# Kernel tuning notes

Measured on AMD Instinct MI355X. Metric: run time of the kernel, lower is better.

Reference implementation:

```python
import jax, jax.numpy as jnp
import numpy as np

N_NODES = 100_000
N_EDGES = 3_200_000
VOCAB = 50_000
D = 256
L_GNN = 4
L_LIN = 2
OUT = 10          # label_size=10 -> output_size=10
N_TGT = 8192
EPS = 1e-5


def layer_norm(x, g, b):
    mu = jnp.mean(x, axis=-1, keepdims=True)
    var = jnp.mean((x - mu) ** 2, axis=-1, keepdims=True)
    return (x - mu) * jax.lax.rsqrt(var + EPS) * g + b


def gcn_conv(x, src, dst, W, b, n):
    # PyG GCNConv defaults: add self loops, symmetric D^-1/2 (A+I) D^-1/2 norm
    h = x @ W                                   # [n, D]
    loops = jnp.arange(n, dtype=src.dtype)
    src2 = jnp.concatenate([src, loops])        # [E+n]
    dst2 = jnp.concatenate([dst, loops])
    deg = jax.ops.segment_sum(jnp.ones(src2.shape[0], dtype=h.dtype), dst2, n)
    dinv = jnp.where(deg > 0, jax.lax.rsqrt(deg), 0.0)
    norm = dinv[src2] * dinv[dst2]              # [E+n]
    out = jax.ops.segment_sum(h[src2] * norm[:, None], dst2, n)  # [n, D]
    return out + b


def setup_inputs() -> dict:
    key = jax.random.key(0)
    ks = jax.random.split(key, 16)
    tokens = jax.random.randint(ks[0], (N_NODES,), 0, VOCAB, dtype=jnp.int32)
    edges = jax.random.randint(ks[1], (2, N_EDGES), 0, N_NODES, dtype=jnp.int32)
    target_indices = jax.random.randint(ks[2], (N_TGT,), 0, N_NODES, dtype=jnp.int32)
    s = 0.05
    emb_table = jax.random.normal(ks[3], (VOCAB, D), jnp.float32)
    gnn_W = jax.random.normal(ks[4], (L_GNN, D, D), jnp.float32) * s
    gnn_b = jnp.zeros((L_GNN, D), jnp.float32)
    gnn_gamma = jnp.ones((L_GNN, D), jnp.float32)
    gnn_beta = jnp.zeros((L_GNN, D), jnp.float32)
    lin_W = jax.random.normal(ks[5], (L_LIN, D, D), jnp.float32) * s
    lin_b = jnp.zeros((L_LIN, D), jnp.float32)
    lin_gamma = jnp.ones((L_LIN, D), jnp.float32)
    lin_beta = jnp.zeros((L_LIN, D), jnp.float32)
    out_W = jax.random.normal(ks[6], (D, OUT), jnp.float32) * s
    out_b = jnp.zeros((OUT,), jnp.float32)
    return {"tokens": tokens, "edges": edges, "target_indices": target_indices,
            "emb_table": emb_table, "gnn_W": gnn_W, "gnn_b": gnn_b,
            "gnn_gamma": gnn_gamma, "gnn_beta": gnn_beta,
            "lin_W": lin_W, "lin_b": lin_b, "lin_gamma": lin_gamma,
            "lin_beta": lin_beta, "out_W": out_W, "out_b": out_b}


def reference(tokens, edges, target_indices, emb_table, gnn_W, gnn_b,
              gnn_gamma, gnn_beta, lin_W, lin_b, lin_gamma, lin_beta,
              out_W, out_b):
    x = emb_table[tokens]                       # [N, D] embedding lookup
    src, dst = edges[0], edges[1]
    for i in range(L_GNN):
        x = gcn_conv(x, src, dst, gnn_W[i], gnn_b[i], N_NODES)
        x = layer_norm(x, gnn_gamma[i], gnn_beta[i])
        x = jax.nn.relu(x)
    x = x[target_indices]                       # [N_TGT, D]
    for i in range(L_LIN):
        x = x @ lin_W[i] + lin_b[i]
        x = layer_norm(x, lin_gamma[i], lin_beta[i])
        x = jax.nn.relu(x)
    return x @ out_W + out_b                    # [N_TGT, OUT]
```

## Files before the change

kernel.cpp:

```cpp
#include <hip/hip_runtime.h>
#include <hip/hip_fp16.h>

#define NN 100000
#define NE 3200000
#define DD 256
#define NT 8192
#define NOUT 10
#define NBUCK 196
#define CSRP_CAP (NE + NBUCK * 4112 + 64)

typedef unsigned short u16;
typedef unsigned int u32;
typedef unsigned char u8;
typedef __attribute__((ext_vector_type(8))) short bf16x8;
typedef __attribute__((ext_vector_type(4))) float f32x4;
typedef __attribute__((ext_vector_type(4))) unsigned int uint4v;

__device__ __forceinline__ float bf2f(u16 u) {
    union { unsigned int i; float f; } v; v.i = ((unsigned int)u) << 16; return v.f;
}
__device__ __forceinline__ u16 f2bf(float f) {
    union { float f; unsigned int i; } v; v.f = f;
    unsigned int x = v.i;
    return (u16)((x + 0x7fffu + ((x >> 16) & 1u)) >> 16);
}
__device__ __forceinline__ unsigned int pack2(float a, float b) {
    return (unsigned int)f2bf(a) | ((unsigned int)f2bf(b) << 16);
}

__device__ __forceinline__ void gl2lds16(const void* g, void* l) {
    __builtin_amdgcn_global_load_lds(
        (const __attribute__((address_space(1))) unsigned int*)g,
        (__attribute__((address_space(3))) unsigned int*)l, 16, 0, 0);
}

__global__ __launch_bounds__(256) void k_wt(const float* __restrict__ gW,
                                            const float* __restrict__ lW,
                                            u16* __restrict__ Wt,
                                            int* __restrict__ bucketCnt,
                                            float* __restrict__ tq) {
    if (blockIdx.x == 0 && threadIdx.x < NBUCK) bucketCnt[threadIdx.x] = 0;
    if (blockIdx.x == 0 && threadIdx.x < 4) tq[NN * 4 + threadIdx.x] = 0.0f;
    int idx = blockIdx.x * 256 + threadIdx.x;
    int l = idx >> 16;
    int nk = idx & 65535;
    int n = nk >> 8, k = nk & 255;
    float v = (l < 4) ? gW[l * 65536 + k * 256 + n]
                      : lW[(l - 4) * 65536 + k * 256 + n];
    Wt[idx] = f2bf(v);
}

__global__ __launch_bounds__(256) void k_binA(const int* __restrict__ dst,
                                              int* __restrict__ bucketCnt) {
    __shared__ int hist[NBUCK];
    int t = threadIdx.x;
    if (t < NBUCK) hist[t] = 0;
    __syncthreads();
    int base = blockIdx.x * 4096;
#pragma unroll
    for (int i = 0; i < 16; i++) {
        int e = base + i * 256 + t;
        if (e < NE) atomicAdd(&hist[dst[e] >> 9], 1);
    }
    __syncthreads();
    if (t < NBUCK && hist[t] > 0) atomicAdd(&bucketCnt[t], hist[t]);
}

__global__ __launch_bounds__(256) void k_bscan(const int* __restrict__ bucketCnt,
                                               int* __restrict__ bucketOff,
                                               int* __restrict__ bucketCur) {
    __shared__ int s[256];
    int t = threadIdx.x;
    int v = (t < NBUCK) ? bucketCnt[t] : 0;
    s[t] = v;
    __syncthreads();
    for (int o = 1; o < 256; o <<= 1) {
        int a = (t >= o) ? s[t - o] : 0;
        __syncthreads();
        s[t] += a;
        __syncthreads();
    }
    if (t < NBUCK) {
        int ex = s[t] - v;
        bucketOff[t] = ex;
        bucketCur[t] = ex;
    }
    if (t == 0) bucketOff[NBUCK] = NE;
}

__global__ __launch_bounds__(1024) void k_binB(const int* __restrict__ src,
                                               const int* __restrict__ dst,
                                               int* __restrict__ bucketCur,
                                               int* __restrict__ recs) {
    __shared__ int hist[NBUCK];
    __shared__ int gbase[NBUCK];
    int t = threadIdx.x;
    if (t < NBUCK) hist[t] = 0;
    __syncthreads();
    int base = blockIdx.x * 16384;
    int recv[16], bks[16], rnk[16];
#pragma unroll
    for (int i = 0; i < 16; i++) {
        int e = base + i * 1024 + t;
        int bk = -1, rec = 0;
        if (e < NE) {
            int s_ = src[e], d_ = dst[e];
            bk = d_ >> 9;
            rec = (s_ << 9) | (d_ & 511);
        }
        bks[i] = bk; recv[i] = rec;
    }
#pragma unroll
    for (int i = 0; i < 16; i++)
        rnk[i] = (bks[i] >= 0) ? atomicAdd(&hist[bks[i]], 1) : 0;
    __syncthreads();
    if (t < NBUCK) {
        int c = hist[t];
        gbase[t] = (c > 0) ? atomicAdd(&bucketCur[t], c) : 0;
    }
    __syncthreads();
#pragma unroll
    for (int i = 0; i < 16; i++)
        if (bks[i] >= 0) {
            int pos = gbase[bks[i]] + rnk[i];
            pos = min(max(pos, 0), NE - 1);
            recs[pos] = recv[i];
        }
}

__global__ __launch_bounds__(256) void k_csrA(const int* __restrict__ recs,
                                              const int* __restrict__ bucketOff,
                                              int2* __restrict__ nodeInfo,
                                              float* __restrict__ dinv,
                                              u32* __restrict__ csrp) {
    __shared__ int cnt[512], off[512];
    int b = blockIdx.x, t = threadIdx.x;
    int beg = min(max(bucketOff[b], 0), NE);
    int end = min(max(bucketOff[b + 1], beg), NE);
    int n = end - beg;
    cnt[t] = 0; cnt[t + 256] = 0;
    __syncthreads();
    for (int i = t; i < n; i += 256)
        atomicAdd(&cnt[recs[beg + i] & 511], 1);
    __syncthreads();
    off[t] = (cnt[t] + 8) & ~7;
    off[t + 256] = (cnt[t + 256] + 8) & ~7;
    __syncthreads();
    for (int o = 1; o < 512; o <<= 1) {
        int v0 = (t >= o) ? off[t - o] : 0;
        int v1 = (t + 256 >= o) ? off[t + 256 - o] : 0;
        __syncthreads();
        off[t] += v0; off[t + 256] += v1;
        __syncthreads();
    }
    int base = (beg + b * 4112 + 7) & ~7;
    for (int k = t; k < 512; k += 256) {
        int node = b * 512 + k;
        if (node >= NN) continue;
        int pd = (cnt[k] + 8) & ~7;
        int nbeg = base + off[k] - pd;
        int2 ni; ni.x = nbeg; ni.y = pd;
        nodeInfo[node] = ni;
        dinv[node] = rsqrtf((float)(cnt[k] + 1));
        csrp[nbeg] = (u32)node;
        for (int j = nbeg + 1 + cnt[k]; j < nbeg + pd; j++) csrp[j] = (u32)NN;
    }
}

__global__ __launch_bounds__(256) void k_csrB(const int* __restrict__ recs,
                                              const int* __restrict__ bucketOff,
                                              const int2* __restrict__ nodeInfo,
                                              u32* __restrict__ csrp) {
    __shared__ int cur[512];
    int b = blockIdx.x, t = threadIdx.x;
    cur[t] = 0; cur[t + 256] = 0;
    __syncthreads();
    int beg = min(max(bucketOff[b], 0), NE);
    int end = min(max(bucketOff[b + 1], beg), NE);
    int n = end - beg;
    for (int i = t; i < n; i += 256) {
        int r = recs[beg + i];
        int dlow = r & 511;
        int s = min(max(r >> 9, 0), NN - 1);
        int node = b * 512 + dlow;
        int rk = atomicAdd(&cur[dlow], 1);
        int2 ni = nodeInfo[node];
        int pos = ni.x + 1 + rk;
        pos = min(max(pos, 0), CSRP_CAP - 1);
        csrp[pos] = (u32)s;
    }
}

#define GEMM_EPILOGUE                                                         \
    for (int i = 0; i < 4; i++)                                               \
        for (int j = 0; j < 4; j++) {                                         \
            int col = colBase + wn * 64 + j * 16 + l16;                       \
            for (int r = 0; r < 4; r++) {                                     \
                int row = rowBase + wm * 64 + i * 16 + quad * 4 + r;          \
                if (row < M) C[row * 256 + col] = f2bf(acc[i][j][r]);         \
            }                                                                 \
        }

#define GEMM_COMPUTE(ASRC, BSRC)                                              \
    for (int ks = 0; ks < 2; ks++) {                                          \
        bf16x8 a_frag[4], b_frag[4];                                          \
        for (int i = 0; i < 4; i++) {                                         \
            int r = wm * 64 + i * 16 + l16;                                   \
            int ch = (ks * 4 + quad) ^ (r & 7);                               \
            a_frag[i] = *(const bf16x8*)(&ASRC[r * 64 + ch * 8]);             \
        }                                                                     \
        for (int j = 0; j < 4; j++) {                                         \
            int r = wn * 64 + j * 16 + l16;                                   \
            int ch = (ks * 4 + quad) ^ (r & 7);                               \
            b_frag[j] = *(const bf16x8*)(&BSRC[r * 64 + ch * 8]);             \
        }                                                                     \
        for (int i = 0; i < 4; i++)                                           \
            for (int j = 0; j < 4; j++)                                       \
                acc[i][j] = __builtin_amdgcn_mfma_f32_16x16x32_bf16(          \
                    a_frag[i], b_frag[j], acc[i][j], 0, 0, 0);                \
    }

#define QUANT_EPILOGUE(Q8, TQ)                                                \
    {                                                                         \
        u8* bb = (u8*)As;                          \
        const int gq = blockIdx.y * 2 + wn;                                   \
        for (int i = 0; i < 4; i++) {                                         \
            float m0 = 0.f, m1 = 0.f, m2 = 0.f, m3 = 0.f;                     \
            for (int j = 0; j < 4; j++) {                                     \
                m0 = fmaxf(m0, fabsf(acc[i][j][0]));                          \
                m1 = fmaxf(m1, fabsf(acc[i][j][1]));                          \
                m2 = fmaxf(m2, fabsf(acc[i][j][2]));                          \
                m3 = fmaxf(m3, fabsf(acc[i][j][3]));                          \
            }                                                                 \
            for (int o = 1; o < 16; o <<= 1) {                                \
                m0 = fmaxf(m0, __shfl_xor(m0, o, 64));                        \
                m1 = fmaxf(m1, __shfl_xor(m1, o, 64));                        \
                m2 = fmaxf(m2, __shfl_xor(m2, o, 64));                        \
                m3 = fmaxf(m3, __shfl_xor(m3, o, 64));                        \
            }                                                                 \
            float i0 = m0 > 0.f ? 126.f / m0 : 0.f;                           \
            float i1 = m1 > 0.f ? 126.f / m1 : 0.f;                           \
            float i2 = m2 > 0.f ? 126.f / m2 : 0.f;                           \
            float i3 = m3 > 0.f ? 126.f / m3 : 0.f;                           \
            int row0 = rowBase + wm * 64 + i * 16 + quad * 4;                 \
            if (l16 == 0) {                                                   \
                if (row0 + 0 < M)                                             \
                    TQ[(row0+0)*4+gq] = m0 * (1.f/126.f) * dinv[row0+0];      \
                if (row0 + 1 < M)                                             \
                    TQ[(row0+1)*4+gq] = m1 * (1.f/126.f) * dinv[row0+1];      \
                if (row0 + 2 < M)                                             \
                    TQ[(row0+2)*4+gq] = m2 * (1.f/126.f) * dinv[row0+2];      \
                if (row0 + 3 < M)                                             \
                    TQ[(row0+3)*4+gq] = m3 * (1.f/126.f) * dinv[row0+3];      \
            }                                                                 \
            int rb = (wm * 64 + i * 16 + quad * 4) * 128;                     \
            for (int j = 0; j < 4; j++) {                                     \
                int cb = wn * 64 + j * 16 + l16;                              \
                bb[rb + cb]       = (u8)((int)rintf(acc[i][j][0]*i0) + 128);  \
                bb[rb + 128 + cb] = (u8)((int)rintf(acc[i][j][1]*i1) + 128);  \
                bb[rb + 256 + cb] = (u8)((int)rintf(acc[i][j][2]*i2) + 128);  \
                bb[rb + 384 + cb] = (u8)((int)rintf(acc[i][j][3]*i3) + 128);  \
            }                                                                 \
        }                                                                     \
        __syncthreads();                                                      \
        for (int u = tid; u < 1024; u += 256) {                               \
            int r = u >> 3, c16 = (u & 7) * 16;                               \
            int row = rowBase + r;                                            \
            if (row < M)                                                      \
                *(uint4*)(Q8 + (size_t)row * 256 + colBase + c16) =           \
                    *(const uint4*)(bb + r * 128 + c16);                      \
        }                                                                     \
    }

__global__ __launch_bounds__(256) void k_gemm(const u16* __restrict__ A,
                                              const u16* __restrict__ Bt,
                                              u16* __restrict__ C, int M) {
    __shared__ __align__(16) u16 As[128 * 64];
    __shared__ __align__(16) u16 Bs[128 * 64];
    const int tid = threadIdx.x;
    const int wave = tid >> 6, lane = tid & 63;
    const int wm = wave >> 1, wn = wave & 1;
    const int rowBase = blockIdx.x * 128;
    const int colBase = blockIdx.y * 128;
    const int quad = lane >> 4, l16 = lane & 15;

    f32x4 acc[4][4] = {};

    for (int kk = 0; kk < 4; kk++) {
        int k0 = kk * 64;
#pragma unroll
        for (int i = 0; i < 4; i++) {
            int j = (i * 4 + wave) * 64 + lane;
            int r = j >> 3, c = j & 7;
            int cg = c ^ (r & 7);
            int ga = rowBase + r; if (ga >= M) ga = M - 1;
            gl2lds16(A + (size_t)ga * 256 + k0 + cg * 8,
                     &As[(i * 4 + wave) * 512]);
            gl2lds16(Bt + (size_t)(colBase + r) * 256 + k0 + cg * 8,
                     &Bs[(i * 4 + wave) * 512]);
        }
        __syncthreads();
        GEMM_COMPUTE(As, Bs)
        __syncthreads();
    }
    GEMM_EPILOGUE
}

__global__ __launch_bounds__(256) void k_gemmq(const u16* __restrict__ A,
                                               const u16* __restrict__ Bt,
                                               const float* __restrict__ dinv,
                                               u8* __restrict__ q8,
                                               float* __restrict__ tq, int M) {
    __shared__ __align__(16) u16 As[128 * 64];
    __shared__ __align__(16) u16 Bs[128 * 64];
    const int tid = threadIdx.x;
    const int wave = tid >> 6, lane = tid & 63;
    const int wm = wave >> 1, wn = wave & 1;
    const int rowBase = blockIdx.x * 128;
    const int colBase = blockIdx.y * 128;
    const int quad = lane >> 4, l16 = lane & 15;

    f32x4 acc[4][4] = {};

    for (int kk = 0; kk < 4; kk++) {
        int k0 = kk * 64;
#pragma unroll
        for (int i = 0; i < 4; i++) {
            int j = (i * 4 + wave) * 64 + lane;
            int r = j >> 3, c = j & 7;
            int cg = c ^ (r & 7);
            int ga = rowBase + r; if (ga >= M) ga = M - 1;
            gl2lds16(A + (size_t)ga * 256 + k0 + cg * 8,
                     &As[(i * 4 + wave) * 512]);
            gl2lds16(Bt + (size_t)(colBase + r) * 256 + k0 + cg * 8,
                     &Bs[(i * 4 + wave) * 512]);
        }
        __syncthreads();
        GEMM_COMPUTE(As, Bs)
        __syncthreads();
    }
    QUANT_EPILOGUE(q8, tq)
}

__global__ __launch_bounds__(256) void k_gemm_embq(const int* __restrict__ tokens,
                                                   const float* __restrict__ emb,
                                                   const u16* __restrict__ Bt,
                                                   const float* __restrict__ dinv,
                                                   u8* __restrict__ q8,
                                                   float* __restrict__ tq, int M) {
    __shared__ __align__(16) u16 As[128 * 64];
    __shared__ __align__(16) u16 Bs[128 * 64];
    __shared__ int tokLDS[128];
    const int tid = threadIdx.x;
    const int wave = tid >> 6, lane = tid & 63;
    const int wm = wave >> 1, wn = wave & 1;
    const int rowBase = blockIdx.x * 128;
    const int colBase = blockIdx.y * 128;
    const int quad = lane >> 4, l16 = lane & 15;

    if (tid < 128) {
        int ga = rowBase + tid; if (ga >= M) ga = M - 1;
        tokLDS[tid] = tokens[ga];
    }
    f32x4 acc[4][4] = {};
    __syncthreads();

    for (int kk = 0; kk < 4; kk++) {
        int k0 = kk * 64;
#pragma unroll
        for (int i = 0; i < 4; i++) {
            int j = (i * 4 + wave) * 64 + lane;
            int r = j >> 3, c = j & 7;
            int cg = c ^ (r & 7);
            const float* srcp = emb + (size_t)tokLDS[r] * 256 + k0 + cg * 8;
            float4 f0 = *(const float4*)srcp;
            float4 f1 = *(const float4*)(srcp + 4);
            uint4 pk;
            pk.x = pack2(f0.x, f0.y); pk.y = pack2(f0.z, f0.w);
            pk.z = pack2(f1.x, f1.y); pk.w = pack2(f1.z, f1.w);
            *(uint4*)(&As[j * 8]) = pk;
            gl2lds16(Bt + (size_t)(colBase + r) * 256 + k0 + cg * 8,
                     &Bs[(i * 4 + wave) * 512]);
        }
        __syncthreads();
        GEMM_COMPUTE(As, Bs)
        __syncthreads();
    }
    QUANT_EPILOGUE(q8, tq)
}

__global__ __launch_bounds__(256) void k_gemm_gather(const u16* __restrict__ X,
                                                     const int* __restrict__ tgt,
                                                     const u16* __restrict__ Bt,
                                                     u16* __restrict__ C, int M) {
    __shared__ __align__(16) u16 As[128 * 64];
    __shared__ __align__(16) u16 Bs[128 * 64];
    __shared__ int rowLDS[128];
    const int tid = threadIdx.x;
    const int wave = tid >> 6, lane = tid & 63;
    const int wm = wave >> 1, wn = wave & 1;
    const int rowBase = blockIdx.x * 128;
    const int colBase = blockIdx.y * 128;
    const int quad = lane >> 4, l16 = lane & 15;

    if (tid < 128) {
        int ga = rowBase + tid; if (ga >= M) ga = M - 1;
        rowLDS[tid] = tgt[ga];
    }
    f32x4 acc[4][4] = {};
    __syncthreads();

    for (int kk = 0; kk < 4; kk++) {
        int k0 = kk * 64;
#pragma unroll
        for (int i = 0; i < 4; i++) {
            int j = (i * 4 + wave) * 64 + lane;
            int r = j >> 3, c = j & 7;
            int cg = c ^ (r & 7);
            uint4 v = *(const uint4*)(X + (size_t)rowLDS[r] * 256 + k0 + cg * 8);
            *(uint4*)(&As[j * 8]) = v;
            gl2lds16(Bt + (size_t)(colBase + r) * 256 + k0 + cg * 8,
                     &Bs[(i * 4 + wave) * 512]);
        }
        __syncthreads();
        GEMM_COMPUTE(As, Bs)
        __syncthreads();
    }
    GEMM_EPILOGUE
}

#define GF8(RR, Q0, Q1, Q2, Q3, W0, W1, W2, W3)                               \
    {                                                                         \
        int s0 = (int)RR.x, s1 = (int)RR.y, s2 = (int)RR.z, s3 = (int)RR.w;   \
        Q0 = *(const uint2*)(qb + (size_t)s0 * 256);                          \
        Q1 = *(const uint2*)(qb + (size_t)s1 * 256);                          \
        Q2 = *(const uint2*)(qb + (size_t)s2 * 256);                          \
        Q3 = *(const uint2*)(qb + (size_t)s3 * 256);                          \
        W0 = tq[s0 * 4 + sg4]; W1 = tq[s1 * 4 + sg4];                         \
        W2 = tq[s2 * 4 + sg4]; W3 = tq[s3 * 4 + sg4];                         \
    }

#define GC8_ONE(Q, W)                                                         \
    {                                                                         \
        Ks += W;                                                              \
        a0 = fmaf(W, (float)(Q.x & 255u), a0);                                \
        a1 = fmaf(W, (float)((Q.x >> 8) & 255u), a1);                         \
        a2 = fmaf(W, (float)((Q.x >> 16) & 255u), a2);                        \
        a3 = fmaf(W, (float)(Q.x >> 24), a3);                                 \
        a4 = fmaf(W, (float)(Q.y & 255u), a4);                                \
        a5 = fmaf(W, (float)((Q.y >> 8) & 255u), a5);                         \
        a6 = fmaf(W, (float)((Q.y >> 16) & 255u), a6);                        \
        a7 = fmaf(W, (float)(Q.y >> 24), a7);                                 \
    }

__global__ __launch_bounds__(256) void k_aggr(const u8* __restrict__ q8,
                                              const float* __restrict__ tq,
                                              const float* __restrict__ dinv,
                                              const int2* __restrict__ nodeInfo,
                                              const u32* __restrict__ csrp,
                                              const float* __restrict__ bias,
                                              const float* __restrict__ gamma,
                                              const float* __restrict__ beta,
                                              u16* __restrict__ xo) {
    const int wave = threadIdx.x >> 6, lane = threadIdx.x & 63;
    const int half = lane >> 5, l32 = lane & 31;
    const int node = blockIdx.x * 4 + wave;
    const int d8 = l32 * 8;
    const int sg4 = l32 >> 3;
    int2 ni = nodeInfo[node];
    float a0=0,a1=0,a2=0,a3=0,a4=0,a5=0,a6=0,a7=0;
    float Ks = 0.0f;
    const u8* qb = q8 + d8;
    const u32* cp = csrp + ni.x + half * 4;
    const int nrec = ni.y;
    int j = 0;
    for (; j + 16 <= nrec; j += 16, cp += 16) {
        uint4v ra = __builtin_nontemporal_load((const uint4v*)cp);
        uint4v rb = __builtin_nontemporal_load((const uint4v*)(cp + 8));
        uint2 qa0, qa1, qa2, qa3, qb0, qb1, qb2, qb3;
        float wa0, wa1, wa2, wa3, wb0, wb1, wb2, wb3;
        GF8(ra, qa0, qa1, qa2, qa3, wa0, wa1, wa2, wa3);
        GF8(rb, qb0, qb1, qb2, qb3, wb0, wb1, wb2, wb3);
        GC8_ONE(qa0, wa0); GC8_ONE(qa1, wa1);
        GC8_ONE(qa2, wa2); GC8_ONE(qa3, wa3);
        GC8_ONE(qb0, wb0); GC8_ONE(qb1, wb1);
        GC8_ONE(qb2, wb2); GC8_ONE(qb3, wb3);
    }
    if (j < nrec) {
        uint4v ra = __builtin_nontemporal_load((const uint4v*)cp);
        uint2 qa0, qa1, qa2, qa3;
        float wa0, wa1, wa2, wa3;
        GF8(ra, qa0, qa1, qa2, qa3, wa0, wa1, wa2, wa3);
        GC8_ONE(qa0, wa0); GC8_ONE(qa1, wa1);
        GC8_ONE(qa2, wa2); GC8_ONE(qa3, wa3);
    }
    a0 += __shfl_xor(a0, 32, 64); a1 += __shfl_xor(a1, 32, 64);
    a2 += __shfl_xor(a2, 32, 64); a3 += __shfl_xor(a3, 32, 64);
    a4 += __shfl_xor(a4, 32, 64); a5 += __shfl_xor(a5, 32, 64);
    a6 += __shfl_xor(a6, 32, 64); a7 += __shfl_xor(a7, 32, 64);
    Ks += __shfl_xor(Ks, 32, 64);

    float dv = dinv[node];
    float c128 = 128.0f * Ks;
    float4 b0 = *(const float4*)(bias + d8);
    float4 b1 = *(const float4*)(bias + d8 + 4);
    a0 = (a0 - c128) * dv + b0.x; a1 = (a1 - c128) * dv + b0.y;
    a2 = (a2 - c128) * dv + b0.z; a3 = (a3 - c128) * dv + b0.w;
    a4 = (a4 - c128) * dv + b1.x; a5 = (a5 - c128) * dv + b1.y;
    a6 = (a6 - c128) * dv + b1.z; a7 = (a7 - c128) * dv + b1.w;
    float s1 = a0+a1+a2+a3+a4+a5+a6+a7;
    float s2 = a0*a0+a1*a1+a2*a2+a3*a3+a4*a4+a5*a5+a6*a6+a7*a7;
    for (int o = 16; o >= 1; o >>= 1) {
        s1 += __shfl_xor(s1, o, 64);
        s2 += __shfl_xor(s2, o, 64);
    }
    float mean = s1 * (1.0f / 256.0f);
    float var = s2 * (1.0f / 256.0f) - mean * mean;
    float rstd = rsqrtf(var + 1e-5f);
    if (half == 0) {
        float4 g0 = *(const float4*)(gamma + d8);
        float4 g1 = *(const float4*)(gamma + d8 + 4);
        float4 e0 = *(const float4*)(beta + d8);
        float4 e1 = *(const float4*)(beta + d8 + 4);
        float y0 = fmaxf((a0 - mean) * rstd * g0.x + e0.x, 0.0f);
        float y1 = fmaxf((a1 - mean) * rstd * g0.y + e0.y, 0.0f);
        float y2 = fmaxf((a2 - mean) * rstd * g0.z + e0.z, 0.0f);
        float y3 = fmaxf((a3 - mean) * rstd * g0.w + e0.w, 0.0f);
        float y4 = fmaxf((a4 - mean) * rstd * g1.x + e1.x, 0.0f);
        float y5 = fmaxf((a5 - mean) * rstd * g1.y + e1.y, 0.0f);
        float y6 = fmaxf((a6 - mean) * rstd * g1.z + e1.z, 0.0f);
        float y7 = fmaxf((a7 - mean) * rstd * g1.w + e1.w, 0.0f);
        uint4v o;
        o.x = pack2(y0, y1);
        o.y = pack2(y2, y3);
        o.z = pack2(y4, y5);
        o.w = pack2(y6, y7);
        __builtin_nontemporal_store(o, (uint4v*)(xo + node * 256 + d8));
    }
}

__global__ __launch_bounds__(256) void k_lnrelu(const u16* __restrict__ h,
                                                const float* __restrict__ bias,
                                                const float* __restrict__ gamma,
                                                const float* __restrict__ beta,
                                                u16* __restrict__ xo) {
    int wave = threadIdx.x >> 6, lane = threadIdx.x & 63;
    int row = blockIdx.x * 4 + wave;
    int base = row * 256 + lane * 4;
    ushort4 hv = *(const ushort4*)(h + base);
    float4 bv = *(const float4*)(bias + lane * 4);
    float a0 = bf2f(hv.x) + bv.x, a1 = bf2f(hv.y) + bv.y;
    float a2 = bf2f(hv.z) + bv.z, a3 = bf2f(hv.w) + bv.w;
    float s1 = a0 + a1 + a2 + a3;
    float s2 = a0 * a0 + a1 * a1 + a2 * a2 + a3 * a3;
    for (int o = 32; o >= 1; o >>= 1) {
        s1 += __shfl_xor(s1, o, 64);
        s2 += __shfl_xor(s2, o, 64);
    }
    float mean = s1 * (1.0f / 256.0f);
    float var = s2 * (1.0f / 256.0f) - mean * mean;
    float rstd = rsqrtf(var + 1e-5f);
    float4 gv = *(const float4*)(gamma + lane * 4);
    float4 be = *(const float4*)(beta + lane * 4);
    float y0 = fmaxf((a0 - mean) * rstd * gv.x + be.x, 0.0f);
    float y1 = fmaxf((a1 - mean) * rstd * gv.y + be.y, 0.0f);
    float y2 = fmaxf((a2 - mean) * rstd * gv.z + be.z, 0.0f);
    float y3 = fmaxf((a3 - mean) * rstd * gv.w + be.w, 0.0f);
    ushort4 o4;
    o4.x = f2bf(y0); o4.y = f2bf(y1); o4.z = f2bf(y2); o4.w = f2bf(y3);
    *(ushort4*)(xo + base) = o4;
}

__global__ __launch_bounds__(256) void k_lnout(const u16* __restrict__ h,
                                               const float* __restrict__ bias,
                                               const float* __restrict__ gamma,
                                               const float* __restrict__ beta,
                                               const float* __restrict__ W,
                                               const float* __restrict__ ob,
                                               float* __restrict__ out) {
    __shared__ float Ws[DD * NOUT];
    int tid = threadIdx.x;
    for (int i = tid; i < DD * NOUT; i += 256) Ws[i] = W[i];
    __syncthreads();
    int wave = tid >> 6, lane = tid & 63;
    int row = blockIdx.x * 4 + wave;
    int base = row * 256 + lane * 4;
    ushort4 hv = *(const ushort4*)(h + base);
    float4 bv = *(const float4*)(bias + lane * 4);
    float a0 = bf2f(hv.x) + bv.x, a1 = bf2f(hv.y) + bv.y;
    float a2 = bf2f(hv.z) + bv.z, a3 = bf2f(hv.w) + bv.w;
    float s1 = a0 + a1 + a2 + a3;
    float s2 = a0 * a0 + a1 * a1 + a2 * a2 + a3 * a3;
    for (int o = 32; o >= 1; o >>= 1) {
        s1 += __shfl_xor(s1, o, 64);
        s2 += __shfl_xor(s2, o, 64);
    }
    float mean = s1 * (1.0f / 256.0f);
    float var = s2 * (1.0f / 256.0f) - mean * mean;
    float rstd = rsqrtf(var + 1e-5f);
    float4 gv = *(const float4*)(gamma + lane * 4);
    float4 be = *(const float4*)(beta + lane * 4);
    float y0 = bf2f(f2bf(fmaxf((a0 - mean) * rstd * gv.x + be.x, 0.0f)));
    float y1 = bf2f(f2bf(fmaxf((a1 - mean) * rstd * gv.y + be.y, 0.0f)));
    float y2 = bf2f(f2bf(fmaxf((a2 - mean) * rstd * gv.z + be.z, 0.0f)));
    float y3 = bf2f(f2bf(fmaxf((a3 - mean) * rstd * gv.w + be.w, 0.0f)));
    int d = lane * 4;
    for (int o = 0; o < NOUT; o++) {
        float p = y0 * Ws[(d + 0) * NOUT + o] + y1 * Ws[(d + 1) * NOUT + o] +
                  y2 * Ws[(d + 2) * NOUT + o] + y3 * Ws[(d + 3) * NOUT + o];
        for (int off = 32; off >= 1; off >>= 1) p += __shfl_xor(p, off, 64);
        if (lane == 0) out[row * NOUT + o] = p + ob[o];
    }
}

extern "C" void kernel_launch(void* const* d_in, const int* in_sizes, int n_in,
                              void* d_out, int out_size, void* d_ws, size_t ws_size,
                              hipStream_t stream) {
    (void)in_sizes; (void)n_in; (void)out_size; (void)ws_size;
    const int* tokens = (const int*)d_in[0];
    const int* edges = (const int*)d_in[1];
    const int* tgt = (const int*)d_in[2];
    const float* emb = (const float*)d_in[3];
    const float* gnn_W = (const float*)d_in[4];
    const float* gnn_b = (const float*)d_in[5];
    const float* gnn_g = (const float*)d_in[6];
    const float* gnn_be = (const float*)d_in[7];
    const float* lin_W = (const float*)d_in[8];
    const float* lin_b = (const float*)d_in[9];
    const float* lin_g = (const float*)d_in[10];
    const float* lin_be = (const float*)d_in[11];
    const float* out_W = (const float*)d_in[12];
    const float* out_b = (const float*)d_in[13];
    float* out = (float*)d_out;

    char* ws = (char*)d_ws;
    u16* x = (u16*)ws;           ws += (size_t)NN * 256 * 2;
    char* hreg = ws;             ws += (size_t)NN * 256 * 2;
    int* recs = (int*)hreg;
    u32* csrp = (u32*)ws;        ws += (size_t)CSRP_CAP * 4;
    int2* nodeInfo = (int2*)ws;  ws += (size_t)NN * 8;
    float* dinv = (float*)ws;    ws += (size_t)NN * 4;
    int* bucketCnt = (int*)ws;   ws += 256 * 4;
    int* bucketOff = (int*)ws;   ws += 256 * 4;
    int* bucketCur = (int*)ws;   ws += 256 * 4;
    u16* Wt = (u16*)ws;          ws += (size_t)6 * 65536 * 2;
    u16* xt = (u16*)ws;          ws += (size_t)NT * 256 * 2;
    u16* ht = (u16*)ws;          ws += (size_t)NT * 256 * 2;
    u8* q8 = (u8*)ws;            ws += (size_t)(NN + 8) * 256;
    float* tq = (float*)ws;      ws += (size_t)(NN + 1) * 16;

    const int* e_src = edges;
    const int* e_dst = edges + NE;

    k_wt<<<1536, 256, 0, stream>>>(gnn_W, lin_W, Wt, bucketCnt, tq);
    k_binA<<<782, 256, 0, stream>>>(e_dst, bucketCnt);
    k_bscan<<<1, 256, 0, stream>>>(bucketCnt, bucketOff, bucketCur);
    k_binB<<<196, 1024, 0, stream>>>(e_src, e_dst, bucketCur, recs);
    k_csrA<<<NBUCK, 256, 0, stream>>>(recs, bucketOff, nodeInfo, dinv, csrp);
    k_csrB<<<NBUCK, 256, 0, stream>>>(recs, bucketOff, nodeInfo, csrp);

    for (int l = 0; l < 4; l++) {
        if (l == 0)
            k_gemm_embq<<<dim3(782, 2), 256, 0, stream>>>(tokens, emb, Wt,
                                                          dinv, q8, tq, NN);
        else
            k_gemmq<<<dim3(782, 2), 256, 0, stream>>>(x, Wt + l * 65536,
                                                      dinv, q8, tq, NN);
        k_aggr<<<25000, 256, 0, stream>>>(q8, tq, dinv, nodeInfo, csrp,
                                          gnn_b + l * 256, gnn_g + l * 256,
                                          gnn_be + l * 256, x);
    }
    k_gemm_gather<<<dim3(64, 2), 256, 0, stream>>>(x, tgt, Wt + 4 * 65536,
                                                   ht, NT);
    k_lnrelu<<<2048, 256, 0, stream>>>(ht, lin_b, lin_g, lin_be, xt);
    k_gemm<<<dim3(64, 2), 256, 0, stream>>>(xt, Wt + 5 * 65536, ht, NT);
    k_lnout<<<2048, 256, 0, stream>>>(ht, lin_b + 256, lin_g + 256,
                                      lin_be + 256, out_W, out_b, out);
}
```

Measured before the change: 1.110 ms.

## Pack fp16 edge norm weights into CSR records and split quant scales per group

Each CSR record now holds the source index in the high 17 bits and a 15-bit fp16 symmetric-normalisation weight dinv[src]*dinv[dst] in the low bits. This removes the dinv multiply in the aggregation epilogue and the per-row dinv folding in the GEMM quant epilogue. Per-row quant scales move from an interleaved [N,4] layout to four planar [4,N] arrays, so each lane group reads its own plane. Padding records become zero-weight entries that point at node 0 instead of a dummy zero row. The trade is fp16 precision on edge weights, plus an extra random dinv[src] read during CSR build.

```diff
diff --git a/kernel.cpp b/kernel.cpp
--- a/kernel.cpp
+++ b/kernel.cpp
@@ -27,6 +27,13 @@
 __device__ __forceinline__ unsigned int pack2(float a, float b) {
     return (unsigned int)f2bf(a) | ((unsigned int)f2bf(b) << 16);
 }
+__device__ __forceinline__ u32 packrec(int src, float w) {
+    unsigned short h = __half_as_ushort(__float2half(w));
+    return ((u32)src << 15) | (u32)(h & 0x7fff);
+}
+__device__ __forceinline__ float recw(u32 r) {
+    return __half2float(__ushort_as_half((unsigned short)(r & 0x7fff)));
+}
 
 __device__ __forceinline__ void gl2lds16(const void* g, void* l) {
     __builtin_amdgcn_global_load_lds(
@@ -37,10 +44,8 @@
 __global__ __launch_bounds__(256) void k_wt(const float* __restrict__ gW,
                                             const float* __restrict__ lW,
                                             u16* __restrict__ Wt,
-                                            int* __restrict__ bucketCnt,
-                                            float* __restrict__ tq) {
+                                            int* __restrict__ bucketCnt) {
     if (blockIdx.x == 0 && threadIdx.x < NBUCK) bucketCnt[threadIdx.x] = 0;
-    if (blockIdx.x == 0 && threadIdx.x < 4) tq[NN * 4 + threadIdx.x] = 0.0f;
     int idx = blockIdx.x * 256 + threadIdx.x;
     int l = idx >> 16;
     int nk = idx & 65535;
@@ -161,15 +166,17 @@
         int nbeg = base + off[k] - pd;
         int2 ni; ni.x = nbeg; ni.y = pd;
         nodeInfo[node] = ni;
-        dinv[node] = rsqrtf((float)(cnt[k] + 1));
-        csrp[nbeg] = (u32)node;
-        for (int j = nbeg + 1 + cnt[k]; j < nbeg + pd; j++) csrp[j] = (u32)NN;
+        float di = rsqrtf((float)(cnt[k] + 1));
+        dinv[node] = di;
+        csrp[nbeg] = packrec(node, di * di);
+        for (int j = nbeg + 1 + cnt[k]; j < nbeg + pd; j++) csrp[j] = 0u;
     }
 }
 
 __global__ __launch_bounds__(256) void k_csrB(const int* __restrict__ recs,
                                               const int* __restrict__ bucketOff,
                                               const int2* __restrict__ nodeInfo,
+                                              const float* __restrict__ dinv,
                                               u32* __restrict__ csrp) {
     __shared__ int cur[512];
     int b = blockIdx.x, t = threadIdx.x;
@@ -185,9 +192,10 @@
         int node = b * 512 + dlow;
         int rk = atomicAdd(&cur[dlow], 1);
         int2 ni = nodeInfo[node];
+        float w = dinv[s] * dinv[node];
         int pos = ni.x + 1 + rk;
         pos = min(max(pos, 0), CSRP_CAP - 1);
-        csrp[pos] = (u32)s;
+        csrp[pos] = packrec(s, w);
     }
 }
 
@@ -220,10 +228,11 @@
                     a_frag[i], b_frag[j], acc[i][j], 0, 0, 0);                \
     }
 
-#define QUANT_EPILOGUE(Q8, TQ)                                                \
+#define QUANT_EPILOGUE(Q8, QS)                                                \
     {                                                                         \
         u8* bb = (u8*)As;                          \
         const int gq = blockIdx.y * 2 + wn;                                   \
+        float* qsp = QS + (size_t)gq * NN;                                    \
         for (int i = 0; i < 4; i++) {                                         \
             float m0 = 0.f, m1 = 0.f, m2 = 0.f, m3 = 0.f;                     \
             for (int j = 0; j < 4; j++) {                                     \
@@ -244,14 +253,10 @@
             float i3 = m3 > 0.f ? 126.f / m3 : 0.f;                           \
             int row0 = rowBase + wm * 64 + i * 16 + quad * 4;                 \
             if (l16 == 0) {                                                   \
-                if (row0 + 0 < M)                                             \
-                    TQ[(row0+0)*4+gq] = m0 * (1.f/126.f) * dinv[row0+0];      \
-                if (row0 + 1 < M)                                             \
-                    TQ[(row0+1)*4+gq] = m1 * (1.f/126.f) * dinv[row0+1];      \
-                if (row0 + 2 < M)                                             \
-                    TQ[(row0+2)*4+gq] = m2 * (1.f/126.f) * dinv[row0+2];      \
-                if (row0 + 3 < M)                                             \
-                    TQ[(row0+3)*4+gq] = m3 * (1.f/126.f) * dinv[row0+3];      \
+                if (row0 + 0 < M) qsp[row0 + 0] = m0 * (1.f / 126.f);         \
+                if (row0 + 1 < M) qsp[row0 + 1] = m1 * (1.f / 126.f);         \
+                if (row0 + 2 < M) qsp[row0 + 2] = m2 * (1.f / 126.f);         \
+                if (row0 + 3 < M) qsp[row0 + 3] = m3 * (1.f / 126.f);         \
             }                                                                 \
             int rb = (wm * 64 + i * 16 + quad * 4) * 128;                     \
             for (int j = 0; j < 4; j++) {                                     \
@@ -308,9 +313,8 @@
 
 __global__ __launch_bounds__(256) void k_gemmq(const u16* __restrict__ A,
                                                const u16* __restrict__ Bt,
-                                               const float* __restrict__ dinv,
                                                u8* __restrict__ q8,
-                                               float* __restrict__ tq, int M) {
+                                               float* __restrict__ qs, int M) {
     __shared__ __align__(16) u16 As[128 * 64];
     __shared__ __align__(16) u16 Bs[128 * 64];
     const int tid = threadIdx.x;
@@ -339,15 +343,14 @@
         GEMM_COMPUTE(As, Bs)
         __syncthreads();
     }
-    QUANT_EPILOGUE(q8, tq)
+    QUANT_EPILOGUE(q8, qs)
 }
 
 __global__ __launch_bounds__(256) void k_gemm_embq(const int* __restrict__ tokens,
                                                    const float* __restrict__ emb,
                                                    const u16* __restrict__ Bt,
-                                                   const float* __restrict__ dinv,
                                                    u8* __restrict__ q8,
-                                                   float* __restrict__ tq, int M) {
+                                                   float* __restrict__ qs, int M) {
     __shared__ __align__(16) u16 As[128 * 64];
     __shared__ __align__(16) u16 Bs[128 * 64];
     __shared__ int tokLDS[128];
@@ -386,7 +389,7 @@
         GEMM_COMPUTE(As, Bs)
         __syncthreads();
     }
-    QUANT_EPILOGUE(q8, tq)
+    QUANT_EPILOGUE(q8, qs)
 }
 
 __global__ __launch_bounds__(256) void k_gemm_gather(const u16* __restrict__ X,
@@ -431,13 +434,14 @@
 
 #define GF8(RR, Q0, Q1, Q2, Q3, W0, W1, W2, W3)                               \
     {                                                                         \
-        int s0 = (int)RR.x, s1 = (int)RR.y, s2 = (int)RR.z, s3 = (int)RR.w;   \
+        int s0 = (int)(RR.x >> 15), s1 = (int)(RR.y >> 15);                   \
+        int s2 = (int)(RR.z >> 15), s3 = (int)(RR.w >> 15);                   \
         Q0 = *(const uint2*)(qb + (size_t)s0 * 256);                          \
         Q1 = *(const uint2*)(qb + (size_t)s1 * 256);                          \
         Q2 = *(const uint2*)(qb + (size_t)s2 * 256);                          \
         Q3 = *(const uint2*)(qb + (size_t)s3 * 256);                          \
-        W0 = tq[s0 * 4 + sg4]; W1 = tq[s1 * 4 + sg4];                         \
-        W2 = tq[s2 * 4 + sg4]; W3 = tq[s3 * 4 + sg4];                         \
+        W0 = recw(RR.x) * qsp[s0]; W1 = recw(RR.y) * qsp[s1];                 \
+        W2 = recw(RR.z) * qsp[s2]; W3 = recw(RR.w) * qsp[s3];                 \
     }
 
 #define GC8_ONE(Q, W)                                                         \
@@ -454,8 +458,7 @@
     }
 
 __global__ __launch_bounds__(256) void k_aggr(const u8* __restrict__ q8,
-                                              const float* __restrict__ tq,
-                                              const float* __restrict__ dinv,
+                                              const float* __restrict__ qs,
                                               const int2* __restrict__ nodeInfo,
                                               const u32* __restrict__ csrp,
                                               const float* __restrict__ bias,
@@ -466,11 +469,11 @@
     const int half = lane >> 5, l32 = lane & 31;
     const int node = blockIdx.x * 4 + wave;
     const int d8 = l32 * 8;
-    const int sg4 = l32 >> 3;
     int2 ni = nodeInfo[node];
     float a0=0,a1=0,a2=0,a3=0,a4=0,a5=0,a6=0,a7=0;
     float Ks = 0.0f;
     const u8* qb = q8 + d8;
+    const float* qsp = qs + (size_t)(l32 >> 3) * NN;
     const u32* cp = csrp + ni.x + half * 4;
     const int nrec = ni.y;
     int j = 0;
@@ -499,15 +502,14 @@
     a4 += __shfl_xor(a4, 32, 64); a5 += __shfl_xor(a5, 32, 64);
     a6 += __shfl_xor(a6, 32, 64); a7 += __shfl_xor(a7, 32, 64);
     Ks += __shfl_xor(Ks, 32, 64);
-
-    float dv = dinv[node];
     float c128 = 128.0f * Ks;
+    a0 -= c128; a1 -= c128; a2 -= c128; a3 -= c128;
+    a4 -= c128; a5 -= c128; a6 -= c128; a7 -= c128;
+
     float4 b0 = *(const float4*)(bias + d8);
     float4 b1 = *(const float4*)(bias + d8 + 4);
-    a0 = (a0 - c128) * dv + b0.x; a1 = (a1 - c128) * dv + b0.y;
-    a2 = (a2 - c128) * dv + b0.z; a3 = (a3 - c128) * dv + b0.w;
-    a4 = (a4 - c128) * dv + b1.x; a5 = (a5 - c128) * dv + b1.y;
-    a6 = (a6 - c128) * dv + b1.z; a7 = (a7 - c128) * dv + b1.w;
+    a0 += b0.x; a1 += b0.y; a2 += b0.z; a3 += b0.w;
+    a4 += b1.x; a5 += b1.y; a6 += b1.z; a7 += b1.w;
     float s1 = a0+a1+a2+a3+a4+a5+a6+a7;
     float s2 = a0*a0+a1*a1+a2*a2+a3*a3+a4*a4+a5*a5+a6*a6+a7*a7;
     for (int o = 16; o >= 1; o >>= 1) {
@@ -646,27 +648,27 @@
     u16* Wt = (u16*)ws;          ws += (size_t)6 * 65536 * 2;
     u16* xt = (u16*)ws;          ws += (size_t)NT * 256 * 2;
     u16* ht = (u16*)ws;          ws += (size_t)NT * 256 * 2;
-    u8* q8 = (u8*)ws;            ws += (size_t)(NN + 8) * 256;
-    float* tq = (float*)ws;      ws += (size_t)(NN + 1) * 16;
+    u8* q8 = (u8*)ws;            ws += (size_t)NN * 256;
+    float* qs = (float*)ws;      ws += (size_t)4 * NN * 4;
 
     const int* e_src = edges;
     const int* e_dst = edges + NE;
 
-    k_wt<<<1536, 256, 0, stream>>>(gnn_W, lin_W, Wt, bucketCnt, tq);
+    k_wt<<<1536, 256, 0, stream>>>(gnn_W, lin_W, Wt, bucketCnt);
     k_binA<<<782, 256, 0, stream>>>(e_dst, bucketCnt);
     k_bscan<<<1, 256, 0, stream>>>(bucketCnt, bucketOff, bucketCur);
     k_binB<<<196, 1024, 0, stream>>>(e_src, e_dst, bucketCur, recs);
     k_csrA<<<NBUCK, 256, 0, stream>>>(recs, bucketOff, nodeInfo, dinv, csrp);
-    k_csrB<<<NBUCK, 256, 0, stream>>>(recs, bucketOff, nodeInfo, csrp);
+    k_csrB<<<NBUCK, 256, 0, stream>>>(recs, bucketOff, nodeInfo, dinv, csrp);
 
     for (int l = 0; l < 4; l++) {
         if (l == 0)
             k_gemm_embq<<<dim3(782, 2), 256, 0, stream>>>(tokens, emb, Wt,
-                                                          dinv, q8, tq, NN);
+                                                          q8, qs, NN);
         else
             k_gemmq<<<dim3(782, 2), 256, 0, stream>>>(x, Wt + l * 65536,
-                                                      dinv, q8, tq, NN);
-        k_aggr<<<25000, 256, 0, stream>>>(q8, tq, dinv, nodeInfo, csrp,
+                                                      q8, qs, NN);
+        k_aggr<<<25000, 256, 0, stream>>>(q8, qs, nodeInfo, csrp,
                                           gnn_b + l * 256, gnn_g + l * 256,
                                           gnn_be + l * 256, x);
     }
```

Measured after the change: 1.087 ms. 1.02x faster.
